# Kernel optimization log

Hardware: AMD Instinct MI355X
Metric: run time of the kernel (lower is better)

Reference implementation:

```python
import jax, jax.numpy as jnp
import numpy as np

KS = 4                                  # kernel_size per axis
K = KS ** 3                             # 64 spatial filter bins
RADIUS = np.float32(1.5 * 6 * 0.025 / 2.0)   # filter_extent / 2 = 0.1125
N_REAL = 20000                          # fluid particles (index N_REAL = far dummy)
E_PAD = 1200000                         # padded edge count


def ball_to_cube(u):
    # volume-preserving unit-ball -> [-1,1]^3 cube map (Griepentrog et al., as in
    # Open3D-ML 'ball_to_cube_volume_preserving'): ball -> cylinder -> cube.
    eps = 1e-9
    x, y, z = u[..., 0], u[..., 1], u[..., 2]
    sq = x * x + y * y + z * z
    norm = jnp.sqrt(sq + eps)
    rxy2 = x * x + y * y
    polar = 1.25 * z * z > rxy2          # top/bottom cone region
    s = jnp.where(polar,
                  jnp.sqrt(3.0 * norm / (norm + jnp.abs(z) + eps)),
                  norm / jnp.sqrt(rxy2 + eps))
    xc = x * s
    yc = y * s
    zc = jnp.where(polar, jnp.sign(z) * norm, 1.5 * z)
    degen = sq < 1e-12
    xc = jnp.where(degen, 0.0, xc)
    yc = jnp.where(degen, 0.0, yc)
    zc = jnp.where(degen, 0.0, zc)
    # cylinder -> cube: inverse concentric (Shirley-Chiu) area-preserving map on xy
    r = jnp.sqrt(xc * xc + yc * yc + eps)
    c1 = jnp.abs(xc) >= jnp.abs(yc)
    xs = jnp.where(jnp.abs(xc) < eps, eps, xc)
    ys = jnp.where(jnp.abs(yc) < eps, eps, yc)
    fop = np.float32(4.0 / np.pi)
    a = jnp.where(c1, jnp.sign(xc) * r, jnp.sign(yc) * r * fop * jnp.arctan(xc / ys))
    b = jnp.where(c1, jnp.sign(xc) * r * fop * jnp.arctan(yc / xs), jnp.sign(yc) * r)
    tiny = (xc * xc + yc * yc) < 1e-12
    a = jnp.where(tiny, 0.0, a)
    b = jnp.where(tiny, 0.0, b)
    return jnp.stack([a, b, zc], axis=-1)


def cconv(feat, pos, src, dst, W, b):
    # ContinuousConv: normalize=False, align_corners=True, linear interpolation,
    # poly6 window on r^2/radius^2, self-neighbors excluded in the edge list.
    offs = (pos[dst] - pos[src]) / RADIUS              # (E,3), inside unit ball
    r2 = jnp.sum(offs * offs, axis=-1)
    win = jnp.clip((1.0 - r2) ** 3, 0.0, 1.0)          # window_poly6; 0 on pad edges
    g = jnp.clip((ball_to_cube(offs) * 0.5 + 0.5) * (KS - 1), 0.0, KS - 1)
    f0f = jnp.floor(g)
    t = g - f0f                                         # trilinear fractions
    f0 = f0f.astype(jnp.int32)
    fj = feat[dst] * win[:, None]                       # (E,Cin) windowed neighbor feats
    n = pos.shape[0]
    cin = feat.shape[1]
    B = jnp.zeros((n * K, cin), feat.dtype)             # per-query per-bin accumulator
    for c in range(8):                                  # 8 trilinear corners
        w = jnp.ones_like(r2)
        kf = jnp.zeros_like(src)
        for ax in range(3):
            bit = (c >> (2 - ax)) & 1
            ia = jnp.minimum(f0[:, ax] + bit, KS - 1)
            w = w * (t[:, ax] if bit else 1.0 - t[:, ax])
            kf = kf * KS + ia
        B = B + jax.ops.segment_sum(fj * w[:, None], src * K + kf, num_segments=n * K)
    out = jnp.einsum('nki,kio->no', B.reshape(n, K, cin), W.reshape(K, cin, -1))
    return out + b


def forward(pos, feats, edge_src, edge_dst, conv0_w, conv0_b, dense0_w, dense0_b,
            conv1_w, conv1_b, dense1_w, dense1_b, conv2_w, conv2_b, dense2_w, dense2_b,
            conv3_w, conv3_b, dense3_w, dense3_b):
    f = jnp.concatenate([jnp.ones_like(pos[:, :1]), feats], axis=-1)   # 13 channels
    x = jnp.concatenate([cconv(f, pos, edge_src, edge_dst, conv0_w, conv0_b),
                         f @ dense0_w + dense0_b], axis=-1)            # 64 + 32 = 96
    layers = [(conv1_w, conv1_b, dense1_w, dense1_b),
              (conv2_w, conv2_b, dense2_w, dense2_b),
              (conv3_w, conv3_b, dense3_w, dense3_b)]
    for cw, cb, dw, db in layers:
        inp = jax.nn.relu(x)
        y = cconv(inp, pos, edge_src, edge_dst, cw, cb) + inp @ dw + db
        x = (y + x) if y.shape[-1] == x.shape[-1] else y               # residual 64->64
    return (x * (1.0 / 128.0))[:N_REAL]                                # pos_correction


def setup_inputs() -> dict:
    rng = np.random.default_rng(0)
    spacing = 0.05                                  # 2 * particle_radius
    g = np.arange(28)
    pts = np.stack(np.meshgrid(g, g, g, indexing='ij'), -1).reshape(-1, 3).astype(np.float64) * spacing
    pts = pts[:N_REAL] + rng.uniform(-0.012, 0.012, (N_REAL, 3))
    # fixed-radius neighbor search, excluding self (radius_search_ignore_query_points)
    r2 = float(RADIUS) ** 2
    sq = (pts ** 2).sum(-1)
    src_l, dst_l = [], []
    for s in range(0, N_REAL, 1000):
        q = pts[s:s + 1000]
        d2 = (q ** 2).sum(-1)[:, None] + sq[None, :] - 2.0 * (q @ pts.T)
        ii, jj = np.nonzero(d2 < r2)
        ii = ii + s
        keep = ii != jj
        src_l.append(ii[keep])
        dst_l.append(jj[keep])
    src = np.concatenate(src_l).astype(np.int32)[:E_PAD]
    dst = np.concatenate(dst_l).astype(np.int32)[:E_PAD]
    pad = E_PAD - src.size
    src = np.concatenate([src, np.zeros(pad, np.int32)])
    dst = np.concatenate([dst, np.full(pad, N_REAL, np.int32)])   # edges to far dummy -> window 0
    pos = np.concatenate([pts, [[1e3, 1e3, 1e3]]], 0).astype(np.float32)
    key = jax.random.key(0)
    ks = jax.random.split(key, 12)
    def w(k, shape, fan_in):
        return jax.random.normal(k, shape, jnp.float32) * np.float32(1.0 / np.sqrt(fan_in))
    return {
        'pos': jnp.asarray(pos),
        'feats': jax.random.normal(ks[0], (N_REAL + 1, 12), jnp.float32),
        'edge_src': jnp.asarray(src),
        'edge_dst': jnp.asarray(dst),
        'conv0_w': w(ks[1], (KS, KS, KS, 13, 64), 13 * 27),
        'conv0_b': jnp.zeros((64,), jnp.float32),
        'dense0_w': w(ks[2], (13, 32), 13),
        'dense0_b': jnp.zeros((32,), jnp.float32),
        'conv1_w': w(ks[3], (KS, KS, KS, 96, 64), 96 * 27),
        'conv1_b': jnp.zeros((64,), jnp.float32),
        'dense1_w': w(ks[4], (96, 64), 96),
        'dense1_b': jnp.zeros((64,), jnp.float32),
        'conv2_w': w(ks[5], (KS, KS, KS, 64, 64), 64 * 27),
        'conv2_b': jnp.zeros((64,), jnp.float32),
        'dense2_w': w(ks[6], (64, 64), 64),
        'dense2_b': jnp.zeros((64,), jnp.float32),
        'conv3_w': w(ks[7], (KS, KS, KS, 64, 3), 64 * 27),
        'conv3_b': jnp.zeros((3,), jnp.float32),
        'dense3_w': w(ks[8], (64, 3), 64),
        'dense3_b': jnp.zeros((3,), jnp.float32),
    }


def reference(pos, feats, edge_src, edge_dst, conv0_w, conv0_b, dense0_w, dense0_b,
              conv1_w, conv1_b, dense1_w, dense1_b, conv2_w, conv2_b, dense2_w, dense2_b,
              conv3_w, conv3_b, dense3_w, dense3_b):
    return forward(pos, feats, edge_src, edge_dst, conv0_w, conv0_b, dense0_w, dense0_b,
                   conv1_w, conv1_b, dense1_w, dense1_b, conv2_w, conv2_b, dense2_w, dense2_b,
                   conv3_w, conv3_b, dense3_w, dense3_b)
```

## Files before the change

### kernel.cpp

```cpp
#include <hip/hip_runtime.h>
#include <math.h>

#define NPTS   20001
#define NREAL  20000
#define EPAD   1200000
#define KK     64
#define RADF   0.1125f

typedef _Float16 half8_t __attribute__((ext_vector_type(8)));
typedef float    floatx4 __attribute__((ext_vector_type(4)));

__device__ __forceinline__ float sgnf(float v){ return v>0.f ? 1.f : (v<0.f ? -1.f : 0.f); }
__device__ __forceinline__ _Float16 lo16(unsigned u){ return __builtin_bit_cast(_Float16, (unsigned short)(u & 0xffffu)); }
__device__ __forceinline__ _Float16 hi16(unsigned u){ return __builtin_bit_cast(_Float16, (unsigned short)(u >> 16)); }
__device__ __forceinline__ unsigned packf(float v){
  _Float16 h = (_Float16)v;
  _Float16 l = (_Float16)(v - (float)h);
  return (unsigned)__builtin_bit_cast(unsigned short, h)
       | ((unsigned)__builtin_bit_cast(unsigned short, l) << 16);
}

__device__ __forceinline__ void* swzp(void* base, int byteoff){
  return (void*)((char*)base + (byteoff ^ (((byteoff >> 6) & 7) << 4)));
}
__device__ __forceinline__ const void* swzp(const void* base, int byteoff){
  return (const void*)((const char*)base + (byteoff ^ (((byteoff >> 6) & 7) << 4)));
}

__global__ void k_find_ereal(const int* __restrict__ dst, int* __restrict__ ereal){
  int lo=0, hi=EPAD;
  while(lo<hi){ int mid=(lo+hi)>>1; if(dst[mid]==NREAL) hi=mid; else lo=mid+1; }
  *ereal = lo;
}

__global__ void k_csr(const int* __restrict__ src, const int* __restrict__ erealp,
                      int* __restrict__ row_start){
  int i = blockIdx.x*blockDim.x + threadIdx.x;
  if(i > NPTS) return;
  int E = *erealp;
  int lo=0, hi=E;
  while(lo<hi){ int mid=(lo+hi)>>1; if(src[mid] < i) lo=mid+1; else hi=mid; }
  row_start[i] = lo;
}

__global__ void k_build_f(const float* __restrict__ feats, float* __restrict__ f){
  int idx = blockIdx.x*blockDim.x + threadIdx.x;
  if(idx >= NPTS*13) return;
  int i = idx/13, c = idx - i*13;
  f[idx] = (c==0) ? 1.f : feats[i*12 + (c-1)];
}

__global__ void k_cvtF(const float* __restrict__ x, unsigned* __restrict__ Fp, int total){
  int idx = blockIdx.x*blockDim.x + threadIdx.x;
  if(idx >= total) return;
  Fp[idx] = packf(fmaxf(x[idx], 0.f));
}

__device__ __forceinline__ void edge_geom(float ox, float oy, float oz,
                                          float& win, float& t0, float& t1, float& t2, int& f0p){
  const float eps = 1e-9f;
  float sq = ox*ox + oy*oy + oz*oz;
  float u = 1.f - sq;
  win = fminf(fmaxf(u*u*u, 0.f), 1.f);
  float norm = sqrtf(sq + eps);
  float rxy2 = ox*ox + oy*oy;
  bool polar = (1.25f*oz*oz > rxy2);
  float s_p = sqrtf(3.f*norm/(norm + fabsf(oz) + eps));
  float s_n = norm / sqrtf(rxy2 + eps);
  float s = polar ? s_p : s_n;
  float xc = ox*s, yc = oy*s;
  float zc = polar ? sgnf(oz)*norm : 1.5f*oz;
  if(sq < 1e-12f){ xc = 0.f; yc = 0.f; zc = 0.f; }
  float r = sqrtf(xc*xc + yc*yc + eps);
  bool c1 = fabsf(xc) >= fabsf(yc);
  float xs = (fabsf(xc) < eps) ? eps : xc;
  float ys = (fabsf(yc) < eps) ? eps : yc;
  const float fop = 1.2732395447351628f;
  float a = c1 ? sgnf(xc)*r : sgnf(yc)*r*fop*atanf(xc/ys);
  float b = c1 ? sgnf(xc)*r*fop*atanf(yc/xs) : sgnf(yc)*r;
  if(xc*xc + yc*yc < 1e-12f){ a = 0.f; b = 0.f; }
  float g0 = fminf(fmaxf((a *0.5f+0.5f)*3.f, 0.f), 3.f);
  float g1 = fminf(fmaxf((b *0.5f+0.5f)*3.f, 0.f), 3.f);
  float g2 = fminf(fmaxf((zc*0.5f+0.5f)*3.f, 0.f), 3.f);
  float f00 = floorf(g0), f01 = floorf(g1), f02 = floorf(g2);
  t0 = g0 - f00; t1 = g1 - f01; t2 = g2 - f02;
  f0p = (int)f00 | ((int)f01 << 2) | ((int)f02 << 4);
}

__global__ __launch_bounds__(256) void k_geom(const float* __restrict__ pos,
    const int* __restrict__ esrc, const int* __restrict__ edst,
    float4* __restrict__ gw, int4* __restrict__ gmz)
{
  int e = blockIdx.x*blockDim.x + threadIdx.x;
  if(e >= EPAD) return;
  const int sn = esrc[e], d = edst[e];
  const float ox = (pos[d*3+0]-pos[sn*3+0])/RADF;
  const float oy = (pos[d*3+1]-pos[sn*3+1])/RADF;
  const float oz = (pos[d*3+2]-pos[sn*3+2])/RADF;
  float win, t0, t1, t2; int f0p;
  edge_geom(ox, oy, oz, win, t0, t1, t2, f0p);
  const int i0 = f0p & 3, i1 = (f0p>>2) & 3, i2 = f0p >> 4;
  const int X0 = i0 << 4, X1 = ((i0+1)&3) << 4;
  const int Y0 = i1 << 2, Y1 = ((i1+1)&3) << 2;
  const int Z0 = i2, Z1 = (i2+1) & 3;
  const float wx0 = win*(1.f-t0), wx1 = win*t0;
  const float wy0 = 1.f-t1, wy1 = t1;
  const float wz0 = 1.f-t2, wz1 = t2;
  gw[e] = make_float4(wx0*wy0, wx0*wy1, wx1*wy0, wx1*wy1);
  const int p0 = Z0 & 1;
  const float zA = p0 ? wz1 : wz0;
  const int   cA = p0 ? Z1 : Z0;
  const int   cB = p0 ? Z0 : Z1;
  const int cells0 = (X0|Y0|cA) | ((X0|Y1|cA)<<8) | ((X1|Y0|cA)<<16) | ((X1|Y1|cA)<<24);
  const int cells1 = (X0|Y0|cB) | ((X0|Y1|cB)<<8) | ((X1|Y0|cB)<<16) | ((X1|Y1|cB)<<24);
  gmz[e] = make_int4(__float_as_int(zA), cells0, cells1, d);
}

template<int OUT3>
__global__ __launch_bounds__(256) void k_scat64m(
    const unsigned* __restrict__ Fp, const float4* __restrict__ gw,
    const int4* __restrict__ gmz, const int* __restrict__ row_start,
    unsigned* __restrict__ B, int node_base,
    const float* __restrict__ W3, float* __restrict__ out)
{
  __shared__ __align__(128) _Float16 Wh[64*32];
  __shared__ __align__(128) _Float16 Wl[64*32];
  __shared__ __align__(128) _Float16 Fh[64*32];
  __shared__ __align__(128) _Float16 Fl[64*32];
  __shared__ __align__(16) float4 Sq[32];
  __shared__ __align__(16) int4   Smd[32];
  __shared__ float red[16];

  const int tid  = threadIdx.x;
  const int node = node_base + blockIdx.x;
  const int wv   = tid >> 6;
  const int lane = tid & 63;
  const int frow = lane & 15;
  const int fb   = (lane >> 4) << 4;

  floatx4 acc[4];
  #pragma unroll
  for(int nt=0;nt<4;++nt){ acc[nt][0]=0.f; acc[nt][1]=0.f; acc[nt][2]=0.f; acc[nt][3]=0.f; }

  half8_t hz;
  #pragma unroll
  for(int q8=0;q8<8;++q8) hz[q8] = (_Float16)0;

  const int e0 = row_start[node], e1 = row_start[node+1];

  for(int eb = e0; eb < e1; eb += 32){
    const int n = (e1 - eb < 32) ? (e1 - eb) : 32;
    __syncthreads();
    if(wv == 0){
      if(lane < 32){
        int ei = eb + lane; if(ei >= e1) ei = e1 - 1;
        Sq[lane]  = gw[ei];
        Smd[lane] = gmz[ei];
      }
    } else {
      for(int j = tid - 64; j < 512; j += 192){
        if(j < 256) ((half8_t*)Wh)[j]       = hz;
        else        ((half8_t*)Wl)[j - 256] = hz;
      }
    }
    __syncthreads();
    {
      half8_t hreg, lreg;
      #pragma unroll
      for(int j=0;j<8;++j){
        const int dst = Smd[wv*8 + j].w;
        const unsigned u = Fp[(size_t)dst*64 + lane];
        hreg[j] = lo16(u);
        lreg[j] = hi16(u);
      }
      *(half8_t*)swzp(Fh, (lane<<6) + (wv<<4)) = hreg;
      *(half8_t*)swzp(Fl, (lane<<6) + (wv<<4)) = lreg;
    }
    if(lane < 8){
      const int ei = wv*8 + lane;
      if(ei < n){
        const float4 q  = Sq[ei];
        const int4   md = Smd[ei];
        const float zA = __int_as_float(md.x), zB = 1.f - zA;
        #pragma unroll
        for(int t=0;t<8;++t){
          const int   cells = (t < 4) ? md.y : md.z;
          const float zz    = (t < 4) ? zA : zB;
          const int   cell  = (cells >> ((t & 3) * 8)) & 255;
          const float qq    = ((t&3)==0) ? q.x : ((t&3)==1) ? q.y : ((t&3)==2) ? q.z : q.w;
          const float wgt   = qq * zz;
          const _Float16 h  = (_Float16)wgt;
          *(_Float16*)swzp(Wh, (cell<<6) + (ei<<1)) = h;
          *(_Float16*)swzp(Wl, (cell<<6) + (ei<<1)) = (_Float16)(wgt - (float)h);
        }
      }
    }
    __syncthreads();
    const half8_t ah = *(const half8_t*)swzp(Wh, ((wv*16 + frow)<<6) + fb);
    const half8_t al = *(const half8_t*)swzp(Wl, ((wv*16 + frow)<<6) + fb);
    #pragma unroll
    for(int nt=0; nt<4; ++nt){
      const half8_t bh = *(const half8_t*)swzp(Fh, ((nt*16 + frow)<<6) + fb);
      const half8_t bl = *(const half8_t*)swzp(Fl, ((nt*16 + frow)<<6) + fb);
      acc[nt] = __builtin_amdgcn_mfma_f32_16x16x32_f16(ah, bh, acc[nt], 0, 0, 0);
      acc[nt] = __builtin_amdgcn_mfma_f32_16x16x32_f16(al, bh, acc[nt], 0, 0, 0);
      acc[nt] = __builtin_amdgcn_mfma_f32_16x16x32_f16(ah, bl, acc[nt], 0, 0, 0);
    }
  }

  if(!OUT3){
    unsigned* Bg = B + (size_t)blockIdx.x*4096;
    #pragma unroll
    for(int nt=0;nt<4;++nt)
      #pragma unroll
      for(int r=0;r<4;++r){
        const int cell = wv*16 + (lane>>4)*4 + r;
        Bg[cell*64 + nt*16 + (lane&15)] = packf(acc[nt][r]);
      }
  } else {
    float s0=0.f, s1=0.f, s2=0.f;
    #pragma unroll
    for(int nt=0;nt<4;++nt){
      #pragma unroll
      for(int r=0;r<4;++r){
        const int cell = wv*16 + (lane>>4)*4 + r;
        const int j3   = (cell*64 + nt*16 + (lane&15)) * 3;
        const float v  = acc[nt][r];
        s0 = fmaf(v, W3[j3+0], s0);
        s1 = fmaf(v, W3[j3+1], s1);
        s2 = fmaf(v, W3[j3+2], s2);
      }
    }
    #pragma unroll
    for(int off = 32; off > 0; off >>= 1){
      s0 += __shfl_down(s0, off);
      s1 += __shfl_down(s1, off);
      s2 += __shfl_down(s2, off);
    }
    if(lane == 0){
      red[wv*4+0] = s0; red[wv*4+1] = s1; red[wv*4+2] = s2;
    }
    __syncthreads();
    if(tid == 0 && node < NREAL){
      out[node*3+0] += (red[0]+red[4]+red[8] +red[12])*(1.f/128.f);
      out[node*3+1] += (red[1]+red[5]+red[9] +red[13])*(1.f/128.f);
      out[node*3+2] += (red[2]+red[6]+red[10]+red[14])*(1.f/128.f);
    }
  }
}

__global__ __launch_bounds__(256) void k_scat96m(
    const unsigned* __restrict__ Fp, const float4* __restrict__ gw,
    const int4* __restrict__ gmz, const int* __restrict__ row_start,
    unsigned* __restrict__ B, int node_base)
{
  __shared__ __align__(128) _Float16 Wh[64*32];
  __shared__ __align__(128) _Float16 Wl[64*32];
  __shared__ __align__(128) _Float16 Fh[96*32];
  __shared__ __align__(128) _Float16 Fl[96*32];
  __shared__ __align__(16) float4 Sq[32];
  __shared__ __align__(16) int4   Smd[32];

  const int tid  = threadIdx.x;
  const int node = node_base + blockIdx.x;
  const int wv   = tid >> 6;
  const int lane = tid & 63;
  const int frow = lane & 15;
  const int fb   = (lane >> 4) << 4;

  floatx4 acc[6];
  #pragma unroll
  for(int nt=0;nt<6;++nt){ acc[nt][0]=0.f; acc[nt][1]=0.f; acc[nt][2]=0.f; acc[nt][3]=0.f; }

  half8_t hz;
  #pragma unroll
  for(int q8=0;q8<8;++q8) hz[q8] = (_Float16)0;

  const int e0 = row_start[node], e1 = row_start[node+1];

  for(int eb = e0; eb < e1; eb += 32){
    const int n = (e1 - eb < 32) ? (e1 - eb) : 32;
    __syncthreads();
    if(wv == 0){
      if(lane < 32){
        int ei = eb + lane; if(ei >= e1) ei = e1 - 1;
        Sq[lane]  = gw[ei];
        Smd[lane] = gmz[ei];
      }
    } else {
      for(int j = tid - 64; j < 512; j += 192){
        if(j < 256) ((half8_t*)Wh)[j]       = hz;
        else        ((half8_t*)Wl)[j - 256] = hz;
      }
    }
    __syncthreads();
    {
      half8_t h0, l0, h1, l1;
      #pragma unroll
      for(int j=0;j<8;++j){
        const int dst = Smd[wv*8 + j].w;
        const unsigned u = Fp[(size_t)dst*96 + lane];
        h0[j] = lo16(u);
        l0[j] = hi16(u);
        if(lane < 32){
          const unsigned u2 = Fp[(size_t)dst*96 + 64 + lane];
          h1[j] = lo16(u2);
          l1[j] = hi16(u2);
        }
      }
      *(half8_t*)swzp(Fh, (lane<<6) + (wv<<4)) = h0;
      *(half8_t*)swzp(Fl, (lane<<6) + (wv<<4)) = l0;
      if(lane < 32){
        *(half8_t*)swzp(Fh, ((64+lane)<<6) + (wv<<4)) = h1;
        *(half8_t*)swzp(Fl, ((64+lane)<<6) + (wv<<4)) = l1;
      }
    }
    if(lane < 8){
      const int ei = wv*8 + lane;
      if(ei < n){
        const float4 q  = Sq[ei];
        const int4   md = Smd[ei];
        const float zA = __int_as_float(md.x), zB = 1.f - zA;
        #pragma unroll
        for(int t=0;t<8;++t){
          const int   cells = (t < 4) ? md.y : md.z;
          const float zz    = (t < 4) ? zA : zB;
          const int   cell  = (cells >> ((t & 3) * 8)) & 255;
          const float qq    = ((t&3)==0) ? q.x : ((t&3)==1) ? q.y : ((t&3)==2) ? q.z : q.w;
          const float wgt   = qq * zz;
          const _Float16 h  = (_Float16)wgt;
          *(_Float16*)swzp(Wh, (cell<<6) + (ei<<1)) = h;
          *(_Float16*)swzp(Wl, (cell<<6) + (ei<<1)) = (_Float16)(wgt - (float)h);
        }
      }
    }
    __syncthreads();
    const half8_t ah = *(const half8_t*)swzp(Wh, ((wv*16 + frow)<<6) + fb);
    const half8_t al = *(const half8_t*)swzp(Wl, ((wv*16 + frow)<<6) + fb);
    #pragma unroll
    for(int nt=0; nt<6; ++nt){
      const half8_t bh = *(const half8_t*)swzp(Fh, ((nt*16 + frow)<<6) + fb);
      const half8_t bl = *(const half8_t*)swzp(Fl, ((nt*16 + frow)<<6) + fb);
      acc[nt] = __builtin_amdgcn_mfma_f32_16x16x32_f16(ah, bh, acc[nt], 0, 0, 0);
      acc[nt] = __builtin_amdgcn_mfma_f32_16x16x32_f16(al, bh, acc[nt], 0, 0, 0);
      acc[nt] = __builtin_amdgcn_mfma_f32_16x16x32_f16(ah, bl, acc[nt], 0, 0, 0);
    }
  }

  unsigned* Bg = B + (size_t)blockIdx.x*6144;
  #pragma unroll
  for(int nt=0;nt<6;++nt)
    #pragma unroll
    for(int r=0;r<4;++r){
      const int cell = wv*16 + (lane>>4)*4 + r;
      Bg[cell*96 + nt*16 + (lane&15)] = packf(acc[nt][r]);
    }
}

__global__ __launch_bounds__(128) void k_scat13(
    const float* __restrict__ feat, const float4* __restrict__ gw,
    const int4* __restrict__ gmz, const int* __restrict__ row_start,
    unsigned* __restrict__ B, int node_base)
{
  constexpr int CIN = 13, BSZ = KK*CIN, ESW = 4, CSTRIDE = BSZ + 8;
  __shared__ __align__(16) float Bl[ESW*CSTRIDE];
  const int tid  = threadIdx.x;
  const int node = node_base + blockIdx.x;

  for(int j = tid; j < ESW*CSTRIDE; j += 128) Bl[j] = 0.f;

  const int e0 = row_start[node], e1 = row_start[node+1];
  const int wv   = tid >> 6;
  const int lane = tid & 63;
  const int slot = lane >> 4;
  const int c    = lane & 15;
  const bool act = (c < CIN);
  float* Bp = Bl + slot*CSTRIDE;
  __syncthreads();

  if(act){
    for(int e = e0 + slot; e < e1; e += ESW){
      const float4 q  = gw[e];
      const int4   md = gmz[e];
      const float zA = __int_as_float(md.x);
      const float z  = wv ? (1.f - zA) : zA;
      const int   cp = wv ? md.z : md.y;
      float v = feat[(size_t)md.w*CIN + c] * z;
      const int b0 = ( cp        & 255)*CIN + c;
      const int b1 = ((cp >> 8)  & 255)*CIN + c;
      const int b2 = ((cp >> 16) & 255)*CIN + c;
      const int b3 = (((unsigned)cp) >> 24)*CIN + c;
      float o0 = Bp[b0], o1 = Bp[b1], o2 = Bp[b2], o3 = Bp[b3];
      o0 = fmaf(q.x, v, o0); o1 = fmaf(q.y, v, o1);
      o2 = fmaf(q.z, v, o2); o3 = fmaf(q.w, v, o3);
      Bp[b0] = o0; Bp[b1] = o1; Bp[b2] = o2; Bp[b3] = o3;
    }
  }
  __syncthreads();

  unsigned* Bg = B + (size_t)blockIdx.x*BSZ;
  for(int j = tid*4; j < BSZ; j += 512){
    float4 a = *(const float4*)&Bl[j];
    #pragma unroll
    for(int k = 1; k < ESW; ++k){
      const float4 t = *(const float4*)&Bl[k*CSTRIDE + j];
      a.x += t.x; a.y += t.y; a.z += t.z; a.w += t.w;
    }
    uint4 o;
    o.x = packf(a.x); o.y = packf(a.y); o.z = packf(a.z); o.w = packf(a.w);
    *(uint4*)&Bg[j] = o;
  }
}

__global__ void k_cvtW(const float* __restrict__ W, _Float16* __restrict__ WhT,
                       _Float16* __restrict__ WlT, int Kd)
{
  int idx = blockIdx.x*blockDim.x + threadIdx.x;
  if(idx >= 64*Kd) return;
  int o = idx / Kd, k = idx - o*Kd;
  float w = W[(size_t)k*64 + o];
  _Float16 h = (_Float16)w;
  WhT[idx] = h;
  WlT[idx] = (_Float16)(w - (float)h);
}

__global__ __launch_bounds__(256) void k_gemm_mfma(
    const unsigned* __restrict__ Ap, const _Float16* __restrict__ WhT,
    const _Float16* __restrict__ WlT, float* __restrict__ P,
    int M, int Kd, int node_base, int ksteps_per)
{
  __shared__ __align__(128) _Float16 Ah[64*32];
  __shared__ __align__(128) _Float16 Al[64*32];
  __shared__ __align__(128) _Float16 Bh[64*32];
  __shared__ __align__(128) _Float16 Blo[64*32];
  const int tid = threadIdx.x;
  const int mbase = blockIdx.x * 64;
  const int s = blockIdx.y;
  const int kt0 = s * ksteps_per * 32;
  const int kt1 = min(Kd, kt0 + ksteps_per*32);
  const int wv = tid >> 6, lane = tid & 63;
  const int row  = tid >> 2;
  const int useg = (tid & 3) * 8;
  const int sb   = (tid & 3) << 4;
  const int frow = lane & 15;
  const int fb   = (lane >> 4) << 4;

  floatx4 acc[4];
  #pragma unroll
  for(int c=0;c<4;++c){ acc[c][0]=0.f; acc[c][1]=0.f; acc[c][2]=0.f; acc[c][3]=0.f; }

  const int grow = mbase + row;
  const unsigned* Arow = (grow < M) ? (Ap + (size_t)grow*Kd) : nullptr;
  const _Float16* WhRow = WhT + (size_t)row*Kd;
  const _Float16* WlRow = WlT + (size_t)row*Kd;

  for(int kt = kt0; kt < kt1; kt += 32){
    unsigned au[8];
    if(Arow){
      *(uint4*)&au[0] = *(const uint4*)(Arow + kt + useg);
      *(uint4*)&au[4] = *(const uint4*)(Arow + kt + useg + 4);
    } else {
      #pragma unroll
      for(int j=0;j<8;++j) au[j] = 0u;
    }
    half8_t hv, lv;
    #pragma unroll
    for(int j=0;j<8;++j){
      hv[j] = lo16(au[j]);
      lv[j] = hi16(au[j]);
    }
    half8_t wh = *(const half8_t*)(WhRow + kt + useg);
    half8_t wl = *(const half8_t*)(WlRow + kt + useg);
    __syncthreads();
    *(half8_t*)swzp(Ah,  (row<<6) + sb) = hv;
    *(half8_t*)swzp(Al,  (row<<6) + sb) = lv;
    *(half8_t*)swzp(Bh,  (row<<6) + sb) = wh;
    *(half8_t*)swzp(Blo, (row<<6) + sb) = wl;
    __syncthreads();
    const half8_t ah = *(const half8_t*)swzp(Ah, ((wv*16 + frow)<<6) + fb);
    const half8_t al = *(const half8_t*)swzp(Al, ((wv*16 + frow)<<6) + fb);
    #pragma unroll
    for(int c=0;c<4;++c){
      const half8_t bh = *(const half8_t*)swzp(Bh,  ((c*16 + frow)<<6) + fb);
      const half8_t bl = *(const half8_t*)swzp(Blo, ((c*16 + frow)<<6) + fb);
      acc[c] = __builtin_amdgcn_mfma_f32_16x16x32_f16(ah, bh, acc[c], 0, 0, 0);
      acc[c] = __builtin_amdgcn_mfma_f32_16x16x32_f16(al, bh, acc[c], 0, 0, 0);
      acc[c] = __builtin_amdgcn_mfma_f32_16x16x32_f16(ah, bl, acc[c], 0, 0, 0);
    }
  }

  const int prow0 = mbase + wv*16 + (lane>>4)*4;
  const int pcol  = lane & 15;
  #pragma unroll
  for(int c=0;c<4;++c){
    #pragma unroll
    for(int r=0;r<4;++r){
      const int rr = prow0 + r;
      if(rr < M)
        P[((size_t)s*NPTS + node_base + rr)*64 + c*16 + pcol] = acc[c][r];
    }
  }
}

template<int S>
__global__ void k_combine(const float* __restrict__ P, float* __restrict__ x,
                          int ldout, int colofs)
{
  int idx = blockIdx.x*blockDim.x + threadIdx.x;
  if(idx >= NPTS*16) return;
  int node = idx >> 4, c4 = (idx & 15) * 4;
  float4 s = *(const float4*)(P + (size_t)node*64 + c4);
  #pragma unroll
  for(int k=1;k<S;++k){
    float4 t = *(const float4*)(P + ((size_t)k*NPTS + node)*64 + c4);
    s.x+=t.x; s.y+=t.y; s.z+=t.z; s.w+=t.w;
  }
  float* xp = x + (size_t)node*ldout + colofs + c4;
  float4 o = *(float4*)xp;
  o.x+=s.x; o.y+=s.y; o.z+=s.z; o.w+=s.w;
  *(float4*)xp = o;
}

__global__ void k_dense0(const float* __restrict__ f, const float* __restrict__ dW,
                         const float* __restrict__ db, const float* __restrict__ cb0,
                         float* __restrict__ out)
{
  int idx = blockIdx.x*blockDim.x + threadIdx.x;
  if(idx >= NPTS*96) return;
  int i = idx/96, c = idx - i*96;
  if(c < 64){ out[idx] = cb0[c]; return; }
  int o = c - 64;
  float s = db[o];
  const float* row = f + (size_t)i*13;
  #pragma unroll
  for(int j=0;j<13;++j) s = fmaf(row[j], dW[j*32+o], s);
  out[idx] = s;
}

__global__ void k_dense(const float* __restrict__ in, int cin,
                        const float* __restrict__ dW, const float* __restrict__ db,
                        const float* __restrict__ cb, const float* __restrict__ resid,
                        float* __restrict__ out)
{
  int idx = blockIdx.x*blockDim.x + threadIdx.x;
  if(idx >= NPTS*64) return;
  int i = idx >> 6, o = idx & 63;
  float s = db[o] + cb[o];
  if(resid) s += resid[idx];
  const float* row = in + (size_t)i*cin;
  for(int c=0;c<cin;++c) s = fmaf(fmaxf(row[c],0.f), dW[c*64+o], s);
  out[idx] = s;
}

__global__ void k_dense3(const float* __restrict__ x2, const float* __restrict__ dW,
                         const float* __restrict__ db, const float* __restrict__ cb,
                         float* __restrict__ out)
{
  int idx = blockIdx.x*blockDim.x + threadIdx.x;
  if(idx >= NREAL*3) return;
  int i = idx/3, o = idx - i*3;
  float s = db[o] + cb[o];
  const float* row = x2 + (size_t)i*64;
  for(int c=0;c<64;++c) s = fmaf(fmaxf(row[c],0.f), dW[c*3+o], s);
  out[idx] = s * (1.f/128.f);
}

static inline size_t alup(size_t x){ return (x + 255) & ~(size_t)255; }

static inline int calc_rows(size_t bcap, int cin, int want){
  size_t perrow = (size_t)KK * cin * 4;
  size_t r = (perrow > 0) ? bcap / perrow : 0;
  if(r >= (size_t)want) return want;
  r = (r / 128) * 128;
  if(r < 128) r = 128;
  return (int)r;
}

extern "C" void kernel_launch(void* const* d_in, const int* in_sizes, int n_in,
                              void* d_out, int out_size, void* d_ws, size_t ws_size,
                              hipStream_t stream)
{
  const float* pos   = (const float*)d_in[0];
  const float* feats = (const float*)d_in[1];
  const int*   esrc  = (const int*)d_in[2];
  const int*   edst  = (const int*)d_in[3];
  const float* c0w = (const float*)d_in[4];
  const float* c0b = (const float*)d_in[5];
  const float* d0w = (const float*)d_in[6];
  const float* d0b = (const float*)d_in[7];
  const float* c1w = (const float*)d_in[8];
  const float* c1b = (const float*)d_in[9];
  const float* d1w = (const float*)d_in[10];
  const float* d1b = (const float*)d_in[11];
  const float* c2w = (const float*)d_in[12];
  const float* c2b = (const float*)d_in[13];
  const float* d2w = (const float*)d_in[14];
  const float* d2b = (const float*)d_in[15];
  const float* c3w = (const float*)d_in[16];
  const float* c3b = (const float*)d_in[17];
  const float* d3w = (const float*)d_in[18];
  const float* d3b = (const float*)d_in[19];
  float* out = (float*)d_out;

  char* w = (char*)d_ws;
  size_t off = 0;
  float* f  = (float*)(w+off); off += alup((size_t)NPTS*13*4);
  float* x0 = (float*)(w+off); off += alup((size_t)NPTS*96*4);
  float* x1 = (float*)(w+off); off += alup((size_t)NPTS*64*4);
  float* x2 = (float*)(w+off); off += alup((size_t)NPTS*64*4);
  int* row_start = (int*)(w+off); off += alup((size_t)(NPTS+1)*4);
  int* ereal = (int*)(w+off);     off += alup(16);
  float4* gw = (float4*)(w+off);  off += alup((size_t)EPAD*16);
  int4*  gmz = (int4*)(w+off);    off += alup((size_t)EPAD*16);
  float* P  = (float*)(w+off); off += alup((size_t)8*NPTS*64*4);
  _Float16* whT = (_Float16*)(w+off); off += alup((size_t)64*6144*2);
  _Float16* wlT = (_Float16*)(w+off); off += alup((size_t)64*6144*2);
  unsigned* Fp0 = (unsigned*)(w+off); off += alup((size_t)NPTS*96*4);
  unsigned* Fp1 = (unsigned*)(w+off); off += alup((size_t)NPTS*64*4);
  unsigned* B = (unsigned*)(w+off);
  size_t bcap = (ws_size > off) ? (ws_size - off) : 0;

  k_find_ereal<<<1,1,0,stream>>>(edst, ereal);
  k_csr<<<(NPTS+1+255)/256,256,0,stream>>>(esrc, ereal, row_start);
  k_build_f<<<(NPTS*13+255)/256,256,0,stream>>>(feats, f);
  k_geom<<<(EPAD+255)/256,256,0,stream>>>(pos, esrc, edst, gw, gmz);

  k_dense0<<<(NPTS*96+255)/256,256,0,stream>>>(f, d0w, d0b, c0b, x0);
  {
    k_cvtW<<<(64*832+255)/256,256,0,stream>>>(c0w, whT, wlT, 832);
    int rows = calc_rows(bcap, 13, 8192);
    for(int base = 0; base < NPTS; base += rows){
      int m = (NPTS - base < rows) ? (NPTS - base) : rows;
      k_scat13<<<m,128,0,stream>>>(f, gw, gmz, row_start, B, base);
      k_gemm_mfma<<<dim3((m+63)/64, 8),256,0,stream>>>(B, whT, wlT, P, m, 832, base, 4);
    }
    k_combine<8><<<(NPTS*16+255)/256,256,0,stream>>>(P, x0, 96, 0);
  }

  k_dense<<<(NPTS*64+255)/256,256,0,stream>>>(x0, 96, d1w, d1b, c1b, nullptr, x1);
  {
    k_cvtW<<<(64*6144+255)/256,256,0,stream>>>(c1w, whT, wlT, 6144);
    k_cvtF<<<(NPTS*96+255)/256,256,0,stream>>>(x0, Fp0, NPTS*96);
    int rows = calc_rows(bcap, 96, 4096);
    for(int base = 0; base < NPTS; base += rows){
      int m = (NPTS - base < rows) ? (NPTS - base) : rows;
      k_scat96m<<<m,256,0,stream>>>(Fp0, gw, gmz, row_start, B, base);
      k_gemm_mfma<<<dim3((m+63)/64, 8),256,0,stream>>>(B, whT, wlT, P, m, 6144, base, 24);
    }
    k_combine<8><<<(NPTS*16+255)/256,256,0,stream>>>(P, x1, 64, 0);
  }

  k_dense<<<(NPTS*64+255)/256,256,0,stream>>>(x1, 64, d2w, d2b, c2b, x1, x2);
  {
    k_cvtW<<<(64*4096+255)/256,256,0,stream>>>(c2w, whT, wlT, 4096);
    k_cvtF<<<(NPTS*64+255)/256,256,0,stream>>>(x1, Fp1, NPTS*64);
    int rows = calc_rows(bcap, 64, 4096);
    for(int base = 0; base < NPTS; base += rows){
      int m = (NPTS - base < rows) ? (NPTS - base) : rows;
      k_scat64m<0><<<m,256,0,stream>>>(Fp1, gw, gmz, row_start, B, base, nullptr, nullptr);
      k_gemm_mfma<<<dim3((m+63)/64, 8),256,0,stream>>>(B, whT, wlT, P, m, 4096, base, 16);
    }
    k_combine<8><<<(NPTS*16+255)/256,256,0,stream>>>(P, x2, 64, 0);
  }

  k_dense3<<<(NREAL*3+255)/256,256,0,stream>>>(x2, d3w, d3b, c3b, out);
  k_cvtF<<<(NPTS*64+255)/256,256,0,stream>>>(x2, Fp1, NPTS*64);
  k_scat64m<1><<<NPTS,256,0,stream>>>(Fp1, gw, gmz, row_start, nullptr, 0, c3w, out);
}
```

Baseline: 977.1 us.

## Fuse dense layers into conv MFMA GEMM by appending node features as extra K

Measured after the change: 883.9 us. 1.11x faster.

```diff
diff --git a/kernel.cpp b/kernel.cpp
--- a/kernel.cpp
+++ b/kernel.cpp
@@ -209,7 +209,7 @@
   }
 
   if(!OUT3){
-    unsigned* Bg = B + (size_t)blockIdx.x*4096;
+    unsigned* Bg = B + (size_t)blockIdx.x*4160;
     #pragma unroll
     for(int nt=0;nt<4;++nt)
       #pragma unroll
@@ -217,6 +217,7 @@
         const int cell = wv*16 + (lane>>4)*4 + r;
         Bg[cell*64 + nt*16 + (lane&15)] = packf(acc[nt][r]);
       }
+    if(tid < 64) Bg[4096 + tid] = Fp[(size_t)node*64 + tid];
   } else {
     float s0=0.f, s1=0.f, s2=0.f;
     #pragma unroll
@@ -347,7 +348,7 @@
     }
   }
 
-  unsigned* Bg = B + (size_t)blockIdx.x*6144;
+  unsigned* Bg = B + (size_t)blockIdx.x*6240;
   #pragma unroll
   for(int nt=0;nt<6;++nt)
     #pragma unroll
@@ -355,6 +356,7 @@
       const int cell = wv*16 + (lane>>4)*4 + r;
       Bg[cell*96 + nt*16 + (lane&15)] = packf(acc[nt][r]);
     }
+  if(tid < 96) Bg[6144 + tid] = Fp[(size_t)node*96 + tid];
 }
 
 __global__ __launch_bounds__(128) void k_scat13(
@@ -413,15 +415,27 @@
 }
 
 __global__ void k_cvtW(const float* __restrict__ W, _Float16* __restrict__ WhT,
-                       _Float16* __restrict__ WlT, int Kd)
-{
-  int idx = blockIdx.x*blockDim.x + threadIdx.x;
-  if(idx >= 64*Kd) return;
-  int o = idx / Kd, k = idx - o*Kd;
+                       _Float16* __restrict__ WlT, int Kcnv, int Ktot)
+{
+  int idx = blockIdx.x*blockDim.x + threadIdx.x;
+  if(idx >= 64*Kcnv) return;
+  int o = idx / Kcnv, k = idx - o*Kcnv;
   float w = W[(size_t)k*64 + o];
   _Float16 h = (_Float16)w;
-  WhT[idx] = h;
-  WlT[idx] = (_Float16)(w - (float)h);
+  WhT[(size_t)o*Ktot + k] = h;
+  WlT[(size_t)o*Ktot + k] = (_Float16)(w - (float)h);
+}
+
+__global__ void k_cvtWd(const float* __restrict__ dW, _Float16* __restrict__ WhT,
+                        _Float16* __restrict__ WlT, int Kcin, int Ktot, int koff)
+{
+  int idx = blockIdx.x*blockDim.x + threadIdx.x;
+  if(idx >= 64*Kcin) return;
+  int o = idx / Kcin, c = idx - o*Kcin;
+  float w = dW[(size_t)c*64 + o];
+  _Float16 h = (_Float16)w;
+  WhT[(size_t)o*Ktot + koff + c] = h;
+  WlT[(size_t)o*Ktot + koff + c] = (_Float16)(w - (float)h);
 }
 
 __global__ __launch_bounds__(256) void k_gemm_mfma(
@@ -537,18 +551,14 @@
   out[idx] = s;
 }
 
-__global__ void k_dense(const float* __restrict__ in, int cin,
-                        const float* __restrict__ dW, const float* __restrict__ db,
-                        const float* __restrict__ cb, const float* __restrict__ resid,
-                        float* __restrict__ out)
+__global__ void k_bias(const float* __restrict__ db, const float* __restrict__ cb,
+                       const float* __restrict__ resid, float* __restrict__ out)
 {
   int idx = blockIdx.x*blockDim.x + threadIdx.x;
   if(idx >= NPTS*64) return;
-  int i = idx >> 6, o = idx & 63;
+  int o = idx & 63;
   float s = db[o] + cb[o];
   if(resid) s += resid[idx];
-  const float* row = in + (size_t)i*cin;
-  for(int c=0;c<cin;++c) s = fmaf(fmaxf(row[c],0.f), dW[c*64+o], s);
   out[idx] = s;
 }
 
@@ -567,8 +577,8 @@
 
 static inline size_t alup(size_t x){ return (x + 255) & ~(size_t)255; }
 
-static inline int calc_rows(size_t bcap, int cin, int want){
-  size_t perrow = (size_t)KK * cin * 4;
+static inline int calc_rows(size_t bcap, int u32row, int want){
+  size_t perrow = (size_t)u32row * 4;
   size_t r = (perrow > 0) ? bcap / perrow : 0;
   if(r >= (size_t)want) return want;
   r = (r / 128) * 128;
@@ -613,8 +623,8 @@
   float4* gw = (float4*)(w+off);  off += alup((size_t)EPAD*16);
   int4*  gmz = (int4*)(w+off);    off += alup((size_t)EPAD*16);
   float* P  = (float*)(w+off); off += alup((size_t)8*NPTS*64*4);
-  _Float16* whT = (_Float16*)(w+off); off += alup((size_t)64*6144*2);
-  _Float16* wlT = (_Float16*)(w+off); off += alup((size_t)64*6144*2);
+  _Float16* whT = (_Float16*)(w+off); off += alup((size_t)64*6400*2);
+  _Float16* wlT = (_Float16*)(w+off); off += alup((size_t)64*6400*2);
   unsigned* Fp0 = (unsigned*)(w+off); off += alup((size_t)NPTS*96*4);
   unsigned* Fp1 = (unsigned*)(w+off); off += alup((size_t)NPTS*64*4);
   unsigned* B = (unsigned*)(w+off);
@@ -627,8 +637,8 @@
 
   k_dense0<<<(NPTS*96+255)/256,256,0,stream>>>(f, d0w, d0b, c0b, x0);
   {
-    k_cvtW<<<(64*832+255)/256,256,0,stream>>>(c0w, whT, wlT, 832);
-    int rows = calc_rows(bcap, 13, 8192);
+    k_cvtW<<<(64*832+255)/256,256,0,stream>>>(c0w, whT, wlT, 832, 832);
+    int rows = calc_rows(bcap, 832, 8192);
     for(int base = 0; base < NPTS; base += rows){
       int m = (NPTS - base < rows) ? (NPTS - base) : rows;
       k_scat13<<<m,128,0,stream>>>(f, gw, gmz, row_start, B, base);
@@ -637,28 +647,30 @@
     k_combine<8><<<(NPTS*16+255)/256,256,0,stream>>>(P, x0, 96, 0);
   }
 
-  k_dense<<<(NPTS*64+255)/256,256,0,stream>>>(x0, 96, d1w, d1b, c1b, nullptr, x1);
+  k_bias<<<(NPTS*64+255)/256,256,0,stream>>>(d1b, c1b, nullptr, x1);
   {
-    k_cvtW<<<(64*6144+255)/256,256,0,stream>>>(c1w, whT, wlT, 6144);
+    k_cvtW<<<(64*6144+255)/256,256,0,stream>>>(c1w, whT, wlT, 6144, 6240);
+    k_cvtWd<<<(64*96+255)/256,256,0,stream>>>(d1w, whT, wlT, 96, 6240, 6144);
     k_cvtF<<<(NPTS*96+255)/256,256,0,stream>>>(x0, Fp0, NPTS*96);
-    int rows = calc_rows(bcap, 96, 4096);
+    int rows = calc_rows(bcap, 6240, 4096);
     for(int base = 0; base < NPTS; base += rows){
       int m = (NPTS - base < rows) ? (NPTS - base) : rows;
       k_scat96m<<<m,256,0,stream>>>(Fp0, gw, gmz, row_start, B, base);
-      k_gemm_mfma<<<dim3((m+63)/64, 8),256,0,stream>>>(B, whT, wlT, P, m, 6144, base, 24);
+      k_gemm_mfma<<<dim3((m+63)/64, 8),256,0,stream>>>(B, whT, wlT, P, m, 6240, base, 25);
     }
     k_combine<8><<<(NPTS*16+255)/256,256,0,stream>>>(P, x1, 64, 0);
   }
 
-  k_dense<<<(NPTS*64+255)/256,256,0,stream>>>(x1, 64, d2w, d2b, c2b, x1, x2);
+  k_bias<<<(NPTS*64+255)/256,256,0,stream>>>(d2b, c2b, x1, x2);
   {
-    k_cvtW<<<(64*4096+255)/256,256,0,stream>>>(c2w, whT, wlT, 4096);
+    k_cvtW<<<(64*4096+255)/256,256,0,stream>>>(c2w, whT, wlT, 4096, 4160);
+    k_cvtWd<<<(64*64+255)/256,256,0,stream>>>(d2w, whT, wlT, 64, 4160, 4096);
     k_cvtF<<<(NPTS*64+255)/256,256,0,stream>>>(x1, Fp1, NPTS*64);
-    int rows = calc_rows(bcap, 64, 4096);
+    int rows = calc_rows(bcap, 4160, 4096);
     for(int base = 0; base < NPTS; base += rows){
       int m = (NPTS - base < rows) ? (NPTS - base) : rows;
       k_scat64m<0><<<m,256,0,stream>>>(Fp1, gw, gmz, row_start, B, base, nullptr, nullptr);
-      k_gemm_mfma<<<dim3((m+63)/64, 8),256,0,stream>>>(B, whT, wlT, P, m, 4096, base, 16);
+      k_gemm_mfma<<<dim3((m+63)/64, 8),256,0,stream>>>(B, whT, wlT, P, m, 4160, base, 17);
     }
     k_combine<8><<<(NPTS*16+255)/256,256,0,stream>>>(P, x2, 64, 0);
   }
```
